# Kernel tuning notes

Measured on AMD Instinct MI355X. Metric: run time of the kernel, lower is better.

## Reference

```python
import jax, jax.numpy as jnp
import numpy as np

N = 100000      # num nodes
M = 25000       # num hyperedges
E = 600000      # num incidences (node, hyperedge) pairs
D_IN, D_HID, D_OUT = 128, 128, 128


def setup_inputs() -> dict:
    key = jax.random.key(0)
    ks = jax.random.split(key, 9)
    s_in = 1.0 / np.sqrt(D_IN)
    s_hid = 1.0 / np.sqrt(D_HID)
    return {
        "x": jax.random.normal(ks[0], (N, D_IN), dtype=jnp.float32),
        "W1": jax.random.normal(ks[1], (D_IN, D_HID), dtype=jnp.float32) * s_in,
        "b1": jnp.zeros((D_HID,), dtype=jnp.float32),
        "W2": jax.random.normal(ks[2], (D_HID, D_HID), dtype=jnp.float32) * s_hid,
        "b2": jnp.zeros((D_HID,), dtype=jnp.float32),
        "W3": jax.random.normal(ks[3], (D_HID, D_OUT), dtype=jnp.float32) * s_hid,
        "b3": jnp.zeros((D_OUT,), dtype=jnp.float32),
        "node_idx": jax.random.randint(ks[4], (E,), 0, N, dtype=jnp.int32),
        "hedge_idx": jax.random.randint(ks[5], (E,), 0, M, dtype=jnp.int32),
        "num_hyperedges": M,
    }


def _hypergraph_conv(x, W, b, node_idx, hedge_idx, num_hyperedges):
    """PyG HypergraphConv (use_attention=False, hyperedge_weight=1):
    out = D^-1 H B^-1 H^T (x @ W) + b
    """
    n = x.shape[0]
    x = x @ W                                   # [N, F_out]
    ones = jnp.ones(node_idx.shape[0], dtype=x.dtype)
    deg_n = jax.ops.segment_sum(ones, node_idx, num_segments=n)              # D
    deg_e = jax.ops.segment_sum(ones, hedge_idx, num_segments=num_hyperedges)  # B
    d_inv = jnp.where(deg_n > 0, 1.0 / deg_n, 0.0)
    b_inv = jnp.where(deg_e > 0, 1.0 / deg_e, 0.0)
    # node -> hyperedge: m_e = B^-1 sum_{i in e} x_i
    m = jax.ops.segment_sum(x[node_idx], hedge_idx, num_segments=num_hyperedges)
    m = m * b_inv[:, None]
    # hyperedge -> node: out_i = D^-1 sum_{e ni i} m_e
    out = jax.ops.segment_sum(m[hedge_idx], node_idx, num_segments=n)
    out = out * d_inv[:, None]
    return out + b


def reference(x, W1, b1, W2, b2, W3, b3, node_idx, hedge_idx, num_hyperedges):
    # dropout is identity in eval mode (training=False)
    x = jax.nn.elu(_hypergraph_conv(x, W1, b1, node_idx, hedge_idx, num_hyperedges))
    x = jax.nn.elu(_hypergraph_conv(x, W2, b2, node_idx, hedge_idx, num_hyperedges))
    x = jax.nn.elu(_hypergraph_conv(x, W3, b3, node_idx, hedge_idx, num_hyperedges))
    return x
```

## Files before the change

### kernel.cpp

```cpp
#include <hip/hip_runtime.h>

#define NN 100000
#define MM 25000
#define EE 600000
#define TT (MM + NN)

#define CVT_BLOCKS 12500
#define NB 782
#define CAP 2048
#define TILE_E 4096
#define GA ((EE + TILE_E - 1) / TILE_E)

typedef __attribute__((ext_vector_type(8))) short short8;
typedef __attribute__((ext_vector_type(4))) float floatx4;

__device__ __forceinline__ float bl(unsigned int u){ return __uint_as_float(u << 16); }
__device__ __forceinline__ float bh(unsigned int u){ return __uint_as_float(u & 0xffff0000u); }
__device__ __forceinline__ unsigned int packbf2(float a, float b){
    unsigned int ua = __float_as_uint(a), ub = __float_as_uint(b);
    ua = (ua + 0x7fffu + ((ua >> 16) & 1u)) >> 16;
    ub = (ub + 0x7fffu + ((ub >> 16) & 1u)) & 0xffff0000u;
    return ua | ub;
}
__device__ __forceinline__ unsigned short f2bf(float f){
    unsigned int u = __float_as_uint(f);
    return (unsigned short)((u + 0x7fffu + ((u >> 16) & 1u)) >> 16);
}
__device__ __forceinline__ void acc8(float* a, uint4 v){
    a[0] += bl(v.x); a[1] += bh(v.x);
    a[2] += bl(v.y); a[3] += bh(v.y);
    a[4] += bl(v.z); a[5] += bh(v.z);
    a[6] += bl(v.w); a[7] += bh(v.w);
}

__global__ __launch_bounds__(256) void k_fused(const float* __restrict__ x, unsigned int* __restrict__ xb,
                        const float* __restrict__ W1, const float* __restrict__ W2,
                        const float* __restrict__ W3, unsigned short* __restrict__ WT,
                        const int* __restrict__ nidx, const int* __restrict__ hidx,
                        int* __restrict__ gcur, unsigned int* __restrict__ items) {
    __shared__ int h[NB];
    __shared__ int cur[NB];
    int b = blockIdx.x;
    int t = threadIdx.x;
    if (b < GA) {
        for (int i = t; i < NB; i += 256) h[i] = 0;
        __syncthreads();
        int base = b * TILE_E;
        #pragma unroll
        for (int k = 0; k < 16; k++) {
            int e = base + k * 256 + t;
            if (e < EE) {
                atomicAdd(&h[hidx[e] >> 6], 1);
                atomicAdd(&h[391 + (nidx[e] >> 8)], 1);
            }
        }
        __syncthreads();
        for (int i = t; i < NB; i += 256) {
            int c = h[i];
            cur[i] = c ? (i * CAP + atomicAdd(&gcur[i], c)) : 0;
        }
        __syncthreads();
        #pragma unroll
        for (int k = 0; k < 16; k++) {
            int e = base + k * 256 + t;
            if (e < EE) {
                int hh = hidx[e], nn = nidx[e];
                int p1 = atomicAdd(&cur[hh >> 6], 1);
                items[p1] = ((unsigned)(hh & 63) << 17) | (unsigned)nn;
                int p2 = atomicAdd(&cur[391 + (nn >> 8)], 1);
                items[p2] = ((unsigned)(nn & 255) << 15) | (unsigned)hh;
            }
        }
    } else if (b < GA + CVT_BLOCKS) {
        int i = (b - GA) * 256 + t;
        float4 v = ((const float4*)x)[i];
        uint2 o; o.x = packbf2(v.x, v.y); o.y = packbf2(v.z, v.w);
        ((uint2*)xb)[i] = o;
    } else {
        int l = b - GA - CVT_BLOCKS;
        const float* W = l == 0 ? W1 : (l == 1 ? W2 : W3);
        unsigned short* T = WT + l * 16384;
        for (int i = t; i < 16384; i += 256) {
            int k = i >> 7, c = i & 127;
            T[c * 128 + k] = f2bf(W[k * 128 + c]);
        }
    }
}

__global__ __launch_bounds__(256) void k_passB(unsigned int* __restrict__ items,
                                               const int* __restrict__ gcur,
                                               int2* __restrict__ ptr2, float* __restrict__ inv,
                                               int* __restrict__ chist) {
    __shared__ unsigned int led[CAP];
    __shared__ unsigned int grp[CAP];
    __shared__ int bins[256], cur[256], tmp[256];
    __shared__ int chs[32];
    int b = blockIdx.x, t = threadIdx.x;
    int base = b * CAP, cnt = gcur[b];
    bool he = b < 391;
    int nbins = he ? 64 : 256;
    int keybase = he ? b * 64 : MM + (b - 391) * 256;
    int shift = he ? 17 : 15;
    unsigned int mask = he ? 0x1FFFFu : 0x7FFFu;
    int keylim = he ? MM : TT;

    for (int i = t; i < cnt; i += 256) led[i] = items[base + i];
    bins[t] = 0;
    if (t < 32) chs[t] = 0;
    __syncthreads();
    for (int i = t; i < cnt; i += 256) atomicAdd(&bins[led[i] >> shift], 1);
    __syncthreads();
    int v = (t < nbins) ? bins[t] : 0;
    tmp[t] = v;
    __syncthreads();
    for (int o = 1; o < 256; o <<= 1) {
        int u = (t >= o) ? tmp[t - o] : 0;
        __syncthreads();
        tmp[t] += u;
        __syncthreads();
    }
    int excl = tmp[t] - v;
    if (t < nbins) {
        int g = keybase + t;
        if (g < keylim) {
            ptr2[g] = make_int2(base + excl, v);
            inv[g] = v ? 1.f / (float)v : 0.f;
            int cls = min((v + 7) >> 3, 15);
            atomicAdd(&chs[cls + (he ? 0 : 16)], 1);
        }
        cur[t] = excl;
    }
    __syncthreads();
    for (int i = t; i < cnt; i += 256) {
        unsigned int it = led[i];
        int p = atomicAdd(&cur[it >> shift], 1);
        grp[p] = it & mask;
    }
    __syncthreads();
    for (int i = t; i < cnt; i += 256) items[base + i] = grp[i];
    if (t < 32 && chs[t]) atomicAdd(&chist[t], chs[t]);
}

#define SCAT_BLOCKS 128
__global__ __launch_bounds__(256) void k_scatter(const int2* __restrict__ ptr2,
                                                 const int* __restrict__ chist, int* __restrict__ ccur,
                                                 int* __restrict__ perm) {
    __shared__ int off[32];
    __shared__ int lh[32];
    __shared__ int lcur[32];
    int t = threadIdx.x;
    if (t < 32) {
        int side = t >> 4, c = t & 15;
        int s = 0;
        for (int k = 0; k < c; k++) s += chist[side * 16 + k];
        off[t] = s;
        lh[t] = 0;
    }
    __syncthreads();
    const int chunk = (TT + SCAT_BLOCKS - 1) / SCAT_BLOCKS;
    int beg = blockIdx.x * chunk;
    int end = min(beg + chunk, TT);
    for (int g = beg + t; g < end; g += 256) {
        int v = ptr2[g].y;
        int cls = min((v + 7) >> 3, 15);
        atomicAdd(&lh[(g < MM ? 0 : 16) + cls], 1);
    }
    __syncthreads();
    if (t < 32) {
        int c = lh[t];
        lcur[t] = c ? (off[t] + atomicAdd(&ccur[t], c)) : 0;
    }
    __syncthreads();
    for (int g = beg + t; g < end; g += 256) {
        int v = ptr2[g].y;
        int cls = min((v + 7) >> 3, 15);
        bool he = g < MM;
        int slot = atomicAdd(&lcur[(he ? 0 : 16) + cls], 1);
        perm[(he ? 0 : MM) + slot] = he ? g : (g - MM);
    }
}

__device__ __forceinline__ void gather_row8(const unsigned int* __restrict__ X,
                                            const unsigned int* __restrict__ adj,
                                            int beg, int deg, int ql, float* a) {
    int end = beg + deg;
    for (int j = beg; j < end; j += 8) {
        int c = end - j;
        int n[8];
        #pragma unroll
        for (int i = 0; i < 8; i++) n[i] = (i < c) ? (int)adj[j + i] : 0;
        uint4 z = make_uint4(0u, 0u, 0u, 0u);
        uint4 v[8];
        #pragma unroll
        for (int i = 0; i < 8; i++) {
            v[i] = z;
            if (i < c) v[i] = *((const uint4*)(X + (unsigned)n[i] * 64u) + ql);
        }
        #pragma unroll
        for (int i = 0; i < 8; i++) acc8(a, v[i]);
    }
}

__global__ __launch_bounds__(256) void k_hegemm(const unsigned int* __restrict__ X,
        const int2* __restrict__ ptr2, const unsigned int* __restrict__ adj,
        const float* __restrict__ b_inv, const unsigned short* __restrict__ WT,
        const int* __restrict__ hperm, unsigned short* __restrict__ C) {
    __shared__ unsigned int tile[16 * 68];
    __shared__ int prow[16];
    int t = threadIdx.x;
    int qidx = t >> 4, ql = t & 15;
    int r0 = blockIdx.x * 16;
    int r = r0 + qidx;
    float a[8] = {0.f,0.f,0.f,0.f,0.f,0.f,0.f,0.f};
    float sc = 0.f;
    if (r < MM) {
        int rt = hperm[r];
        if (ql == 0) prow[qidx] = rt;
        int2 pe = ptr2[rt];
        gather_row8(X, adj, pe.x, pe.y, ql, a);
        sc = b_inv[rt];
    } else if (ql == 0) {
        prow[qidx] = -1;
    }
    uint4 o;
    o.x = packbf2(a[0] * sc, a[1] * sc);
    o.y = packbf2(a[2] * sc, a[3] * sc);
    o.z = packbf2(a[4] * sc, a[5] * sc);
    o.w = packbf2(a[6] * sc, a[7] * sc);
    *((uint4*)(tile + qidx * 68 + ql * 4)) = o;
    __syncthreads();

    int wv = t >> 6, lane = t & 63;
    int mm = lane & 15, quad = lane >> 4;
    floatx4 acc0 = (floatx4){0.f,0.f,0.f,0.f}, acc1 = acc0;
    int c0 = wv * 2;
    #pragma unroll
    for (int q = 0; q < 4; q++) {
        short8 af = *reinterpret_cast<const short8*>((const short*)(tile + mm * 68) + q * 32 + quad * 8);
        short8 b0 = *reinterpret_cast<const short8*>(WT + (c0 * 16 + mm) * 128 + q * 32 + quad * 8);
        short8 b1 = *reinterpret_cast<const short8*>(WT + ((c0 + 1) * 16 + mm) * 128 + q * 32 + quad * 8);
        acc0 = __builtin_amdgcn_mfma_f32_16x16x32_bf16(af, b0, acc0, 0, 0, 0);
        acc1 = __builtin_amdgcn_mfma_f32_16x16x32_bf16(af, b1, acc1, 0, 0, 0);
    }
    #pragma unroll
    for (int rg = 0; rg < 4; rg++) {
        int rr = prow[quad * 4 + rg];
        if (rr >= 0) {
            C[rr * 128 + c0 * 16 + mm]       = f2bf(acc0[rg]);
            C[rr * 128 + (c0 + 1) * 16 + mm] = f2bf(acc1[rg]);
        }
    }
}

template<bool F32OUT>
__global__ __launch_bounds__(256) void k_gather_nd(const unsigned int* __restrict__ X,
        const int2* __restrict__ ptr2, const unsigned int* __restrict__ adj,
        const float* __restrict__ d_inv, const float* __restrict__ bias,
        const int* __restrict__ nperm, void* __restrict__ out) {
    int gw = (blockIdx.x * 256 + threadIdx.x) >> 6;
    int lane = threadIdx.x & 63, quad = lane >> 4, ql = lane & 15;
    int r = gw * 4 + quad;
    if (r >= NN) return;
    int rt = nperm[r];
    int2 pe = ptr2[rt];
    float a[8] = {0.f,0.f,0.f,0.f,0.f,0.f,0.f,0.f};
    gather_row8(X, adj, pe.x, pe.y, ql, a);
    float sc = d_inv[rt];
    const float4* b4 = (const float4*)bias;
    float4 bA = b4[ql * 2], bB = b4[ql * 2 + 1];
    float f[8];
    f[0] = a[0] * sc + bA.x; f[1] = a[1] * sc + bA.y;
    f[2] = a[2] * sc + bA.z; f[3] = a[3] * sc + bA.w;
    f[4] = a[4] * sc + bB.x; f[5] = a[5] * sc + bB.y;
    f[6] = a[6] * sc + bB.z; f[7] = a[7] * sc + bB.w;
    #pragma unroll
    for (int i = 0; i < 8; i++) f[i] = f[i] > 0.f ? f[i] : __expf(f[i]) - 1.f;
    if (F32OUT) {
        float* o = (float*)out + (unsigned)rt * 128u;
        ((float4*)o)[ql * 2]     = make_float4(f[0], f[1], f[2], f[3]);
        ((float4*)o)[ql * 2 + 1] = make_float4(f[4], f[5], f[6], f[7]);
    } else {
        uint4 o4;
        o4.x = packbf2(f[0], f[1]); o4.y = packbf2(f[2], f[3]);
        o4.z = packbf2(f[4], f[5]); o4.w = packbf2(f[6], f[7]);
        ((uint4*)((unsigned int*)out + (unsigned)rt * 64u))[ql] = o4;
    }
}

extern "C" void kernel_launch(void* const* d_in, const int* in_sizes, int n_in,
                              void* d_out, int out_size, void* d_ws, size_t ws_size,
                              hipStream_t stream) {
    const float* x  = (const float*)d_in[0];
    const float* W1 = (const float*)d_in[1];
    const float* b1 = (const float*)d_in[2];
    const float* W2 = (const float*)d_in[3];
    const float* b2 = (const float*)d_in[4];
    const float* W3 = (const float*)d_in[5];
    const float* b3 = (const float*)d_in[6];
    const int* nidx = (const int*)d_in[7];
    const int* hidx = (const int*)d_in[8];

    char* ws = (char*)d_ws;
    size_t o = 0;
    auto alloc = [&](size_t b) -> char* { char* p = ws + o; o = (o + b + 255) & ~(size_t)255; return p; };
    int2*  ptr2  = (int2*)alloc((size_t)TT * 8);
    float* invq  = (float*)alloc(TT * 4);
    int*   gcur  = (int*)alloc((NB + 64) * 4);
    unsigned int* items = (unsigned int*)alloc((size_t)NB * CAP * 4);
    unsigned short* WT   = (unsigned short*)alloc(3 * 128 * 128 * 2);
    unsigned short* mbuf = (unsigned short*)alloc((size_t)MM * 128 * 2);
    int* perm = (int*)alloc((size_t)TT * 4);
    int* chist = gcur + NB;
    int* ccur  = chist + 32;

    unsigned int* xb   = (unsigned int*)d_out;
    unsigned int* bufA = (unsigned int*)d_out;
    unsigned int* bufB = (unsigned int*)d_out + (size_t)NN * 64;

    hipMemsetAsync(gcur, 0, (NB + 64) * 4, stream);
    k_fused<<<GA + CVT_BLOCKS + 3, 256, 0, stream>>>(x, xb, W1, W2, W3, WT, nidx, hidx, gcur, items);
    k_passB<<<NB, 256, 0, stream>>>(items, gcur, ptr2, invq, chist);
    k_scatter<<<SCAT_BLOCKS, 256, 0, stream>>>(ptr2, chist, ccur, perm);

    const float* b_inv = invq;
    const float* d_inv = invq + MM;
    const int2* nptr2 = ptr2 + MM;
    const int* hperm = perm;
    const int* nperm = perm + MM;
    const int grid_hg = (MM + 15) / 16;
    const int grid_nd = NN / 16;
    const unsigned int* adj = items;

    k_hegemm<<<grid_hg, 256, 0, stream>>>(xb, ptr2, adj, b_inv, WT, hperm, mbuf);
    k_gather_nd<false><<<grid_nd, 256, 0, stream>>>((const unsigned int*)mbuf, nptr2, adj, d_inv, b1, nperm, (void*)bufA);
    k_hegemm<<<grid_hg, 256, 0, stream>>>(bufA, ptr2, adj, b_inv, WT + 16384, hperm, mbuf);
    k_gather_nd<false><<<grid_nd, 256, 0, stream>>>((const unsigned int*)mbuf, nptr2, adj, d_inv, b2, nperm, (void*)bufB);
    k_hegemm<<<grid_hg, 256, 0, stream>>>(bufB, ptr2, adj, b_inv, WT + 32768, hperm, mbuf);
    k_gather_nd<true ><<<grid_nd, 256, 0, stream>>>((const unsigned int*)mbuf, nptr2, adj, d_inv, b3, nperm, d_out);
}
```

Baseline: 371.6 us.

## Use grid-stride loops for convert and node gather, prefetch adjacency indices

Several changes land together. The bf16 conversion of x now uses 1024 grid-striding blocks that each handle four float4 per thread, replacing 12500 one-shot blocks. The node-side gather kernel becomes a persistent grid-stride loop over 2048 blocks, and the bias loads are hoisted out of the row loop. gather_row8 software-prefetches the next eight adjacency indices while the current eight rows are loaded, and the histogram tile is halved so the binning pass gets more blocks. Together these aim to cut launch and tail overhead and hide index-load latency, at the cost of more registers and possible load imbalance across the persistent waves.

New measurement: 337.3 us. 1.1x faster.

```diff
diff --git a/kernel.cpp b/kernel.cpp
--- a/kernel.cpp
+++ b/kernel.cpp
@@ -5,11 +5,12 @@
 #define EE 600000
 #define TT (MM + NN)
 
-#define CVT_BLOCKS 12500
 #define NB 782
 #define CAP 2048
-#define TILE_E 4096
+#define TILE_E 2048
 #define GA ((EE + TILE_E - 1) / TILE_E)
+#define CVT_B 1024
+#define ND_BLOCKS 2048
 
 typedef __attribute__((ext_vector_type(8))) short short8;
 typedef __attribute__((ext_vector_type(4))) float floatx4;
@@ -47,7 +48,7 @@
         __syncthreads();
         int base = b * TILE_E;
         #pragma unroll
-        for (int k = 0; k < 16; k++) {
+        for (int k = 0; k < TILE_E / 256; k++) {
             int e = base + k * 256 + t;
             if (e < EE) {
                 atomicAdd(&h[hidx[e] >> 6], 1);
@@ -61,7 +62,7 @@
         }
         __syncthreads();
         #pragma unroll
-        for (int k = 0; k < 16; k++) {
+        for (int k = 0; k < TILE_E / 256; k++) {
             int e = base + k * 256 + t;
             if (e < EE) {
                 int hh = hidx[e], nn = nidx[e];
@@ -71,13 +72,25 @@
                 items[p2] = ((unsigned)(nn & 255) << 15) | (unsigned)hh;
             }
         }
-    } else if (b < GA + CVT_BLOCKS) {
-        int i = (b - GA) * 256 + t;
-        float4 v = ((const float4*)x)[i];
-        uint2 o; o.x = packbf2(v.x, v.y); o.y = packbf2(v.z, v.w);
-        ((uint2*)xb)[i] = o;
+    } else if (b < GA + CVT_B) {
+        const int F4 = NN * 32;
+        for (int u = (b - GA) * 1024; u < F4; u += CVT_B * 1024) {
+            float4 v0 = ((const float4*)x)[u + t];
+            float4 v1 = ((const float4*)x)[u + 256 + t];
+            float4 v2 = ((const float4*)x)[u + 512 + t];
+            float4 v3 = ((const float4*)x)[u + 768 + t];
+            uint2 o0, o1, o2, o3;
+            o0.x = packbf2(v0.x, v0.y); o0.y = packbf2(v0.z, v0.w);
+            o1.x = packbf2(v1.x, v1.y); o1.y = packbf2(v1.z, v1.w);
+            o2.x = packbf2(v2.x, v2.y); o2.y = packbf2(v2.z, v2.w);
+            o3.x = packbf2(v3.x, v3.y); o3.y = packbf2(v3.z, v3.w);
+            ((uint2*)xb)[u + t] = o0;
+            ((uint2*)xb)[u + 256 + t] = o1;
+            ((uint2*)xb)[u + 512 + t] = o2;
+            ((uint2*)xb)[u + 768 + t] = o3;
+        }
     } else {
-        int l = b - GA - CVT_BLOCKS;
+        int l = b - GA - CVT_B;
         const float* W = l == 0 ? W1 : (l == 1 ? W2 : W3);
         unsigned short* T = WT + l * 16384;
         for (int i = t; i < 16384; i += 256) {
@@ -183,21 +196,26 @@
 __device__ __forceinline__ void gather_row8(const unsigned int* __restrict__ X,
                                             const unsigned int* __restrict__ adj,
                                             int beg, int deg, int ql, float* a) {
+    if (deg <= 0) return;
     int end = beg + deg;
+    int n[8];
+    #pragma unroll
+    for (int i = 0; i < 8; i++) n[i] = (beg + i < end) ? (int)adj[beg + i] : -1;
     for (int j = beg; j < end; j += 8) {
-        int c = end - j;
-        int n[8];
-        #pragma unroll
-        for (int i = 0; i < 8; i++) n[i] = (i < c) ? (int)adj[j + i] : 0;
-        uint4 z = make_uint4(0u, 0u, 0u, 0u);
+        int jn = j + 8;
+        int m[8];
+        #pragma unroll
+        for (int i = 0; i < 8; i++) m[i] = (jn + i < end) ? (int)adj[jn + i] : -1;
         uint4 v[8];
         #pragma unroll
         for (int i = 0; i < 8; i++) {
-            v[i] = z;
-            if (i < c) v[i] = *((const uint4*)(X + (unsigned)n[i] * 64u) + ql);
+            v[i] = make_uint4(0u, 0u, 0u, 0u);
+            if (n[i] >= 0) v[i] = *((const uint4*)(X + (unsigned)n[i] * 64u) + ql);
         }
         #pragma unroll
         for (int i = 0; i < 8; i++) acc8(a, v[i]);
+        #pragma unroll
+        for (int i = 0; i < 8; i++) n[i] = m[i];
     }
 }
 
@@ -257,33 +275,35 @@
         const int2* __restrict__ ptr2, const unsigned int* __restrict__ adj,
         const float* __restrict__ d_inv, const float* __restrict__ bias,
         const int* __restrict__ nperm, void* __restrict__ out) {
-    int gw = (blockIdx.x * 256 + threadIdx.x) >> 6;
     int lane = threadIdx.x & 63, quad = lane >> 4, ql = lane & 15;
-    int r = gw * 4 + quad;
-    if (r >= NN) return;
-    int rt = nperm[r];
-    int2 pe = ptr2[rt];
-    float a[8] = {0.f,0.f,0.f,0.f,0.f,0.f,0.f,0.f};
-    gather_row8(X, adj, pe.x, pe.y, ql, a);
-    float sc = d_inv[rt];
+    int wave0 = (blockIdx.x * 256 + threadIdx.x) >> 6;
+    const int NWAVES = ND_BLOCKS * 4;
     const float4* b4 = (const float4*)bias;
     float4 bA = b4[ql * 2], bB = b4[ql * 2 + 1];
-    float f[8];
-    f[0] = a[0] * sc + bA.x; f[1] = a[1] * sc + bA.y;
-    f[2] = a[2] * sc + bA.z; f[3] = a[3] * sc + bA.w;
-    f[4] = a[4] * sc + bB.x; f[5] = a[5] * sc + bB.y;
-    f[6] = a[6] * sc + bB.z; f[7] = a[7] * sc + bB.w;
-    #pragma unroll
-    for (int i = 0; i < 8; i++) f[i] = f[i] > 0.f ? f[i] : __expf(f[i]) - 1.f;
-    if (F32OUT) {
-        float* o = (float*)out + (unsigned)rt * 128u;
-        ((float4*)o)[ql * 2]     = make_float4(f[0], f[1], f[2], f[3]);
-        ((float4*)o)[ql * 2 + 1] = make_float4(f[4], f[5], f[6], f[7]);
-    } else {
-        uint4 o4;
-        o4.x = packbf2(f[0], f[1]); o4.y = packbf2(f[2], f[3]);
-        o4.z = packbf2(f[4], f[5]); o4.w = packbf2(f[6], f[7]);
-        ((uint4*)((unsigned int*)out + (unsigned)rt * 64u))[ql] = o4;
+    for (int rq = wave0; rq < NN / 4; rq += NWAVES) {
+        int r = rq * 4 + quad;
+        int rt = nperm[r];
+        int2 pe = ptr2[rt];
+        float a[8] = {0.f,0.f,0.f,0.f,0.f,0.f,0.f,0.f};
+        gather_row8(X, adj, pe.x, pe.y, ql, a);
+        float sc = d_inv[rt];
+        float f[8];
+        f[0] = a[0] * sc + bA.x; f[1] = a[1] * sc + bA.y;
+        f[2] = a[2] * sc + bA.z; f[3] = a[3] * sc + bA.w;
+        f[4] = a[4] * sc + bB.x; f[5] = a[5] * sc + bB.y;
+        f[6] = a[6] * sc + bB.z; f[7] = a[7] * sc + bB.w;
+        #pragma unroll
+        for (int i = 0; i < 8; i++) f[i] = f[i] > 0.f ? f[i] : __expf(f[i]) - 1.f;
+        if (F32OUT) {
+            float* o = (float*)out + (unsigned)rt * 128u;
+            ((float4*)o)[ql * 2]     = make_float4(f[0], f[1], f[2], f[3]);
+            ((float4*)o)[ql * 2 + 1] = make_float4(f[4], f[5], f[6], f[7]);
+        } else {
+            uint4 o4;
+            o4.x = packbf2(f[0], f[1]); o4.y = packbf2(f[2], f[3]);
+            o4.z = packbf2(f[4], f[5]); o4.w = packbf2(f[6], f[7]);
+            ((uint4*)((unsigned int*)out + (unsigned)rt * 64u))[ql] = o4;
+        }
     }
 }
 
@@ -318,7 +338,7 @@
     unsigned int* bufB = (unsigned int*)d_out + (size_t)NN * 64;
 
     hipMemsetAsync(gcur, 0, (NB + 64) * 4, stream);
-    k_fused<<<GA + CVT_BLOCKS + 3, 256, 0, stream>>>(x, xb, W1, W2, W3, WT, nidx, hidx, gcur, items);
+    k_fused<<<GA + CVT_B + 3, 256, 0, stream>>>(x, xb, W1, W2, W3, WT, nidx, hidx, gcur, items);
     k_passB<<<NB, 256, 0, stream>>>(items, gcur, ptr2, invq, chist);
     k_scatter<<<SCAT_BLOCKS, 256, 0, stream>>>(ptr2, chist, ccur, perm);
 
@@ -328,13 +348,12 @@
     const int* hperm = perm;
     const int* nperm = perm + MM;
     const int grid_hg = (MM + 15) / 16;
-    const int grid_nd = NN / 16;
     const unsigned int* adj = items;
 
     k_hegemm<<<grid_hg, 256, 0, stream>>>(xb, ptr2, adj, b_inv, WT, hperm, mbuf);
-    k_gather_nd<false><<<grid_nd, 256, 0, stream>>>((const unsigned int*)mbuf, nptr2, adj, d_inv, b1, nperm, (void*)bufA);
+    k_gather_nd<false><<<ND_BLOCKS, 256, 0, stream>>>((const unsigned int*)mbuf, nptr2, adj, d_inv, b1, nperm, (void*)bufA);
     k_hegemm<<<grid_hg, 256, 0, stream>>>(bufA, ptr2, adj, b_inv, WT + 16384, hperm, mbuf);
-    k_gather_nd<false><<<grid_nd, 256, 0, stream>>>((const unsigned int*)mbuf, nptr2, adj, d_inv, b2, nperm, (void*)bufB);
+    k_gather_nd<false><<<ND_BLOCKS, 256, 0, stream>>>((const unsigned int*)mbuf, nptr2, adj, d_inv, b2, nperm, (void*)bufB);
     k_hegemm<<<grid_hg, 256, 0, stream>>>(bufB, ptr2, adj, b_inv, WT + 32768, hperm, mbuf);
-    k_gather_nd<true ><<<grid_nd, 256, 0, stream>>>((const unsigned int*)mbuf, nptr2, adj, d_inv, b3, nperm, d_out);
-}
+    k_gather_nd<true ><<<ND_BLOCKS, 256, 0, stream>>>((const unsigned int*)mbuf, nptr2, adj, d_inv, b3, nperm, d_out);
+}
```
